# Kernel optimization log

Measured on AMD Instinct MI355X. Metric: run time of the kernel, lower is better.

## Reference

```python
import jax, jax.numpy as jnp
import numpy as np

N_QUBITS = 16
N_LAYERS = 4
DIM = 2 ** N_QUBITS  # 65536 == prod(input_size)


def rot_matrix(phi, theta, omega):
    # PennyLane Rot(phi, theta, omega) = RZ(omega) RY(theta) RZ(phi)
    c = jnp.cos(theta * 0.5).astype(jnp.complex64)
    s = jnp.sin(theta * 0.5).astype(jnp.complex64)
    ep = jnp.exp(-0.5j * (phi + omega).astype(jnp.complex64))  # e^{-i(phi+omega)/2}
    em = jnp.exp(0.5j * (phi - omega).astype(jnp.complex64))   # e^{ i(phi-omega)/2}
    return jnp.stack([
        jnp.stack([ep * c, -em * s]),
        jnp.stack([jnp.conj(em) * s, jnp.conj(ep) * c]),
    ])


def apply_1q(state, U, wire):
    # state: (batch, 2, 2, ..., 2); wire axis is 1 + wire (wire 0 = MSB, PennyLane convention)
    ax = 1 + wire
    s = jnp.moveaxis(state, ax, -1)
    s = jnp.einsum('...j,ij->...i', s, U)
    return jnp.moveaxis(s, -1, ax)


def apply_cnot(state, control, target):
    s = jnp.moveaxis(state, (1 + control, 1 + target), (-2, -1))
    # flip target amplitudes where control bit == 1
    s = jnp.concatenate([s[..., 0:1, :], s[..., 1:2, ::-1]], axis=-2)
    return jnp.moveaxis(s, (-2, -1), (1 + control, 1 + target))


def circuit_expvals(x, weights):
    batch = x.shape[0]
    x = x.reshape(batch, -1)  # (batch, 65536)
    # AmplitudeEmbedding with normalize=True (pad_with=0.0 is a no-op: exactly 2^16 features)
    norm = jnp.sqrt(jnp.sum(x * x, axis=1, keepdims=True))
    state = (x / norm).astype(jnp.complex64).reshape((batch,) + (2,) * N_QUBITS)
    # StronglyEntanglingLayers: per layer, Rot on every wire then a ring of CNOTs with range r
    for l in range(N_LAYERS):
        for w in range(N_QUBITS):
            U = rot_matrix(weights[l, w, 0], weights[l, w, 1], weights[l, w, 2])
            state = apply_1q(state, U, w)
        r = (l % (N_QUBITS - 1)) + 1  # PennyLane default ranges
        for w in range(N_QUBITS):
            state = apply_cnot(state, w, (w + r) % N_QUBITS)
    probs = (state.real ** 2 + state.imag ** 2)  # (batch, 2, ..., 2) float32
    z = []
    for w in range(N_QUBITS):
        p = jnp.moveaxis(probs, 1 + w, 1).reshape(batch, 2, -1).sum(-1)
        z.append(p[:, 0] - p[:, 1])  # <PauliZ(w)>
    return jnp.stack(z, axis=1)  # (batch, n_qubits)


def setup_inputs() -> dict:
    key = jax.random.key(0)
    k1, k2, k3, k4 = jax.random.split(key, 4)
    x = jax.random.normal(k1, (128, 256, 256), dtype=jnp.float32)
    # TorchLayer default init: uniform(0, 2*pi)
    weights = jax.random.uniform(k2, (N_LAYERS, N_QUBITS, 3), dtype=jnp.float32) * (2.0 * np.pi)
    # Linear(16, 2), xavier_uniform weight, default bias init (frozen but still used)
    bound = float(np.sqrt(6.0 / (N_QUBITS + 2)))
    c_weight = jax.random.uniform(k3, (2, N_QUBITS), dtype=jnp.float32, minval=-bound, maxval=bound)
    bb = float(1.0 / np.sqrt(N_QUBITS))
    c_bias = jax.random.uniform(k4, (2,), dtype=jnp.float32, minval=-bb, maxval=bb)
    return {"x": x, "weights": weights, "c_weight": c_weight, "c_bias": c_bias}


def reference(x, weights, c_weight, c_bias):
    expvals = circuit_expvals(x, weights)
    return expvals @ c_weight.T + c_bias  # (batch, 2)
```

## Files before the change

### kernel.cpp

```cpp
#include <hip/hip_runtime.h>
#include <cmath>
#include <utility>
#include <cstddef>


namespace qsim {

constexpr int NQ = 16;
constexpr int NL = 4;
constexpr int NGMAX = 12;
constexpr int GMAX  = 36;
constexpr int BDIM  = 13;
constexpr int CDIM  = 3;

constexpr int parity16(unsigned v) {
    int p = 0;
    for (int k = 0; k < 16; ++k) p ^= (int)((v >> k) & 1u);
    return p;
}
constexpr int topbit(unsigned v) {
    int b = -1;
    for (int k = 0; k < 16; ++k) if ((v >> k) & 1u) b = k;
    return b;
}

struct PlanT {
    int ngroups;
    int ng[NGMAX];
    unsigned char gl[NGMAX][GMAX];
    unsigned char gw[NGMAX][GMAX];
    unsigned short mloc[NGMAX][GMAX];
    unsigned short rloc[NGMAX][GMAX];
    unsigned short grow[NGMAX][GMAX];
    unsigned short V[NGMAX][BDIM];
    unsigned short U[NGMAX][CDIM];
    unsigned short frow[16];
    unsigned short floc[16];
    bool ok;
};

constexpr PlanT make_plan() {
    PlanT P{};
    P.ok = true;

    unsigned col[16] = {}, rowv[16] = {};
    for (int b = 0; b < 16; ++b) { col[b] = 1u << b; rowv[b] = 1u << b; }
    unsigned gmask[64] = {}, growg[64] = {};
    unsigned char glay[64] = {}, gwire[64] = {};
    int gi = 0;
    for (int l = 0; l < NL; ++l) {
        for (int w = 0; w < NQ; ++w) {
            const int b = 15 - w;
            gmask[gi] = col[b]; growg[gi] = rowv[b];
            glay[gi] = (unsigned char)l; gwire[gi] = (unsigned char)w; ++gi;
        }
        const int r = (l % (NQ - 1)) + 1;
        for (int w = 0; w < NQ; ++w) {
            const int cb = 15 - w;
            const int tb = 15 - ((w + r) % NQ);
            col[cb] ^= col[tb];
            rowv[tb] ^= rowv[cb];
        }
    }
    for (int b = 0; b < 16; ++b) P.frow[b] = (unsigned short)rowv[b];

    for (int a = 0; a < 16; ++a)
        for (int b2 = 0; b2 < 16; ++b2)
            if (parity16(rowv[a] & col[b2]) != (a == b2 ? 1 : 0)) P.ok = false;
    for (int i = 0; i < 64; ++i)
        if (parity16(gmask[i] & growg[i]) != 1) P.ok = false;

    bool applied[64] = {};
    int napplied = 0, grp = 0;
    while (napplied < 64) {
        if (grp >= NGMAX) { P.ok = false; break; }
        unsigned B[BDIM] = {}; int piv[BDIM] = {}; int nb = 0;
        for (int i = 0; i < 6; ++i) { B[i] = 1u << i; piv[i] = i; ++nb; }
        unsigned tmask[GMAX] = {}, trow[GMAX] = {};
        int cnt = 0;
        bool progress = true;
        while (progress) {
            progress = false;
            int lay = -1;
            for (int i = 0; i < 64; ++i)
                if (!applied[i]) { lay = glay[i]; break; }
            if (lay < 0) break;
            for (int w = 15; w >= 0; --w) {
                const int idx = lay * 16 + w;
                if (applied[idx]) continue;
                unsigned v = gmask[idx];
                for (int i = 0; i < nb; ++i) if ((v >> piv[i]) & 1u) v ^= B[i];
                if (v != 0u && nb == BDIM) continue;
                if (cnt >= GMAX) { P.ok = false; continue; }
                if (v != 0u) {
                    int pb = 0; while (((v >> pb) & 1u) == 0u) ++pb;
                    for (int i = 0; i < nb; ++i) if ((B[i] >> pb) & 1u) B[i] ^= v;
                    B[nb] = v; piv[nb] = pb; ++nb;
                }
                P.gl[grp][cnt] = glay[idx];
                P.gw[grp][cnt] = gwire[idx];
                tmask[cnt] = gmask[idx]; trow[cnt] = growg[idx];
                ++cnt;
                applied[idx] = true; ++napplied; progress = true;
            }
        }
        for (int bbit = 0; bbit < 16 && nb < BDIM; ++bbit) {
            unsigned v = 1u << bbit;
            for (int i = 0; i < nb; ++i) if ((v >> piv[i]) & 1u) v ^= B[i];
            if (v != 0u) {
                int pb = 0; while (((v >> pb) & 1u) == 0u) ++pb;
                for (int i = 0; i < nb; ++i) if ((B[i] >> pb) & 1u) B[i] ^= v;
                B[nb] = v; piv[nb] = pb; ++nb;
            }
        }
        if (nb != BDIM) P.ok = false;
        for (int i = 1; i < BDIM; ++i) {
            unsigned bv = B[i]; int pv = piv[i]; int j = i - 1;
            while (j >= 0 && B[j] > bv) { B[j+1] = B[j]; piv[j+1] = piv[j]; --j; }
            B[j+1] = bv; piv[j+1] = pv;
        }
        for (int i = 0; i < 6; ++i) if (B[i] != (1u << i)) P.ok = false;
        for (int i = 0; i < BDIM; ++i) P.V[grp][i] = (unsigned short)B[i];
        int cu = 0;
        for (int bbit = 0; bbit < 16; ++bbit) {
            bool isp = false;
            for (int i = 0; i < BDIM; ++i) if (piv[i] == bbit) isp = true;
            if (!isp) { if (cu < CDIM) P.U[grp][cu] = (unsigned short)(1u << bbit); ++cu; }
        }
        if (cu != CDIM) P.ok = false;
        for (int g = 0; g < cnt; ++g) {
            unsigned m = tmask[g], ml = 0;
            for (int i = 0; i < BDIM; ++i)
                if ((m >> piv[i]) & 1u) { ml |= 1u << i; m ^= B[i]; }
            if (m != 0u) P.ok = false;
            if (ml == 0u) P.ok = false;
            P.mloc[grp][g] = (unsigned short)ml;
            unsigned rl = 0;
            for (int i = 0; i < BDIM; ++i)
                rl |= (unsigned)parity16(trow[g] & B[i]) << i;
            P.rloc[grp][g] = (unsigned short)rl;
            P.grow[grp][g] = (unsigned short)trow[g];
        }
        P.ng[grp] = cnt;
        ++grp;
    }
    P.ngroups = grp;
    for (int q = 0; q < 16; ++q) {
        unsigned rl = 0;
        for (int s = 0; s < BDIM; ++s)
            rl |= (unsigned)parity16(P.frow[q] & P.V[P.ngroups - 1][s]) << s;
        P.floc[q] = (unsigned short)rl;
    }
    return P;
}

constexpr PlanT PLAN = make_plan();
static_assert(PLAN.ok, "constexpr plan construction failed");
static_assert(PLAN.ngroups >= 2 && PLAN.ngroups <= NGMAX, "unexpected group count");


__device__ __forceinline__ float xsgn(float v, unsigned sb) {
    return __uint_as_float(__float_as_uint(v) ^ sb);
}

template<int G>
__device__ __forceinline__ unsigned vmid(int tid) {
    unsigned rx = 0;
    if (tid & 64)  rx ^= PLAN.V[G][6];
    if (tid & 128) rx ^= PLAN.V[G][7];
    if (tid & 256) rx ^= PLAN.V[G][8];
    if (tid & 512) rx ^= PLAN.V[G][9];
    return rx;
}
template<int G>
__device__ __forceinline__ unsigned vhi(int j) {
    unsigned rx = 0;
    if (j & 1) rx ^= PLAN.V[G][10];
    if (j & 2) rx ^= PLAN.V[G][11];
    if (j & 4) rx ^= PLAN.V[G][12];
    return rx;
}

template<int G, int g>
__device__ __forceinline__ void apply_gates(float2* tile,
                                            const float* __restrict__ gu,
                                            unsigned base, int tid)
{
    if constexpr (g < PLAN.ng[G]) {
        constexpr unsigned ml  = PLAN.mloc[G][g];
        constexpr unsigned rl  = PLAN.rloc[G][g];
        constexpr unsigned grw = PLAN.grow[G][g];
        constexpr int gidx = PLAN.gl[G][g] * 16 + PLAN.gw[G][g];

        const float* up = gu + gidx * 8;
        const float u0r = up[0], u0i = up[1], u1r = up[2], u1i = up[3];
        const int pgb = __popc(grw & base) & 1;

        if constexpr (ml < 64u) {
            const int prt = (pgb ^ __popc(rl & (unsigned)tid)) & 1;
            #pragma unroll
            for (int j = 0; j < 8; ++j) {
                const int L = (j << 10) | tid;
                const float2 a = tile[L];
                const float bx = __shfl_xor(a.x, (int)ml, 64);
                const float by = __shfl_xor(a.y, (int)ml, 64);
                const int p = prt ^ (__popc(rl & ((unsigned)j << 10)) & 1);
                const unsigned sb = (unsigned)p << 31;
                const float say = xsgn(a.y, sb), sax = xsgn(a.x, sb);
                const float sbx = xsgn(bx, sb),  sby = xsgn(by, sb);
                float2 o;
                o.x = u0r*a.x - u0i*say + u1r*sbx - u1i*by;
                o.y = u0r*a.y + u0i*sax + u1r*sby + u1i*bx;
                tile[L] = o;
            }
        } else {
            constexpr int hb = topbit(ml);
            const unsigned etid = (((unsigned)tid >> hb) << (hb + 1)) |
                                  ((unsigned)tid & ((1u << hb) - 1u));
            const int ptid = (pgb ^ __popc(rl & etid)) & 1;
            #pragma unroll
            for (int j = 0; j < 4; ++j) {
                const unsigned cj = (unsigned)j << 10;
                const unsigned ej = ((cj >> hb) << (hb + 1)) |
                                    (cj & ((1u << hb) - 1u));
                const unsigned i = etid | ej;
                const unsigned k = i ^ ml;
                const float2 a = tile[i];
                const float2 b = tile[k];
                const int p = ptid ^ (__popc(rl & ej) & 1);
                const unsigned sb = (unsigned)p << 31;
                const float say = xsgn(a.y, sb), sax = xsgn(a.x, sb);
                const float sbx = xsgn(b.x, sb), sby = xsgn(b.y, sb);
                float2 oi, ok;
                oi.x = u0r*a.x - u0i*say + u1r*sbx - u1i*b.y;
                oi.y = u0r*a.y + u0i*sax + u1r*sby + u1i*b.x;
                ok.x = u0r*b.x + u0i*sby - u1r*sax - u1i*a.y;
                ok.y = u0r*b.y - u0i*sbx - u1r*say + u1i*a.x;
                tile[i] = oi; tile[k] = ok;
            }
        }
        constexpr bool cur_lane  = (ml < 64u);
        constexpr bool next_lane = (g + 1 < PLAN.ng[G]) &&
                                   (PLAN.mloc[G][g + 1] < 64u);
        constexpr bool last_gate = (g + 1 >= PLAN.ng[G]);
        if constexpr (!(cur_lane && (next_lane || last_gate))) __syncthreads();
        apply_gates<G, g + 1>(tile, gu, base, tid);
    }
}

template<int G, bool FIRST, bool LAST>
__global__ __launch_bounds__(1024, 8)
void pass_kernel(const float* __restrict__ x,
                 const float* __restrict__ gu,
                 float2* __restrict__ state,
                 const float* __restrict__ invn,
                 float* __restrict__ zpart)
{
    __shared__ float2 tile[1 << 13];
    const int tid = (int)threadIdx.x;
    const int batch = (int)blockIdx.x >> 3;
    const unsigned coset = (unsigned)blockIdx.x & 7u;

    unsigned base = 0;
    if (coset & 1u) base ^= PLAN.U[G][0];
    if (coset & 2u) base ^= PLAN.U[G][1];
    if (coset & 4u) base ^= PLAN.U[G][2];
    const unsigned gbt = base ^ (unsigned)(tid & 63) ^ vmid<G>(tid);
    const int boff = batch << 16;

    if constexpr (FIRST) {
        const float inv = invn[batch];
        #pragma unroll
        for (int j = 0; j < 8; ++j)
            tile[(j << 10) | tid] =
                make_float2(x[boff + (int)(gbt ^ vhi<G>(j))] * inv, 0.f);
    } else {
        #pragma unroll
        for (int j = 0; j < 8; ++j)
            tile[(j << 10) | tid] = state[boff + (int)(gbt ^ vhi<G>(j))];
    }
    if constexpr (!(PLAN.ng[G] > 0 && PLAN.mloc[G][0] < 64u)) __syncthreads();

    apply_gates<G, 0>(tile, gu, base, tid);

    if constexpr (LAST) {
        unsigned sbits = 0;
        #pragma unroll
        for (int q = 0; q < 16; ++q) {
            const int s0 = (__popc((unsigned)PLAN.frow[q] & base)
                          + __popc((unsigned)PLAN.floc[q] & (unsigned)tid)) & 1;
            sbits |= (unsigned)s0 << q;
        }
        const int wave = tid >> 6, lane = tid & 63;
        const int W = (int)blockIdx.x * 16 + wave;
        #pragma unroll
        for (int h = 0; h < 2; ++h) {
            float acc[8] = {0,0,0,0,0,0,0,0};
            #pragma unroll
            for (int j = 0; j < 8; ++j) {
                const float2 a = tile[(j << 10) | tid];
                const float pr = a.x*a.x + a.y*a.y;
                #pragma unroll
                for (int q8 = 0; q8 < 8; ++q8) {
                    const int q = h * 8 + q8;
                    const int s = (int)((sbits >> q) & 1u) ^
                        (__popc((unsigned)PLAN.floc[q] & ((unsigned)j << 10)) & 1);
                    acc[q8] += s ? -pr : pr;
                }
            }
            #pragma unroll
            for (int q8 = 0; q8 < 8; ++q8) {
                float v = acc[q8];
                #pragma unroll
                for (int o = 32; o; o >>= 1) v += __shfl_xor(v, o, 64);
                if (lane == 0) zpart[W * 16 + h * 8 + q8] = v;
            }
        }
    } else {
        #pragma unroll
        for (int j = 0; j < 8; ++j)
            state[boff + (int)(gbt ^ vhi<G>(j))] = tile[(j << 10) | tid];
    }
}

__global__ __launch_bounds__(256)
void norm_kernel(const float* __restrict__ x, float* __restrict__ invn)
{
    const int b = (int)blockIdx.x;
    const float4* xv = reinterpret_cast<const float4*>(x + ((size_t)b << 16));
    float s = 0.f;
    for (int i = (int)threadIdx.x; i < 16384; i += 256) {
        const float4 v = xv[i];
        s += v.x*v.x + v.y*v.y + v.z*v.z + v.w*v.w;
    }
    #pragma unroll
    for (int o = 32; o; o >>= 1) s += __shfl_xor(s, o, 64);
    __shared__ float partial[4];
    if ((threadIdx.x & 63u) == 0u) partial[threadIdx.x >> 6] = s;
    __syncthreads();
    if (threadIdx.x == 0) {
        const float t = partial[0] + partial[1] + partial[2] + partial[3];
        invn[b] = 1.0f / sqrtf(t);
    }
}

__global__ void gateu_kernel(const float* __restrict__ wts, float* __restrict__ gu)
{
    const int i = (int)threadIdx.x;
    if (i < 64) {
        const float phi = wts[i*3+0], th = wts[i*3+1], om = wts[i*3+2];
        float sh, ch; sincosf(0.5f * th, &sh, &ch);
        float sap, cap; sincosf(0.5f * (phi + om), &sap, &cap);
        float sam, cam; sincosf(0.5f * (phi - om), &sam, &cam);
        gu[i*8+0] =  cap*ch;  gu[i*8+1] = -sap*ch;
        gu[i*8+2] = -cam*sh;  gu[i*8+3] = -sam*sh;
        gu[i*8+4] =  cam*sh;  gu[i*8+5] = -sam*sh;
        gu[i*8+6] =  cap*ch;  gu[i*8+7] =  sap*ch;
    }
}

__global__ __launch_bounds__(1024)
void out_kernel(const float* __restrict__ zpart, const float* __restrict__ cw,
                const float* __restrict__ cb, float* __restrict__ out)
{
    const int b = (int)blockIdx.x;
    const int q = (int)(threadIdx.x >> 6);
    const int c = (int)(threadIdx.x & 63u);
    float v = zpart[(size_t)(((b << 7) | c) * 16 + q)]
            + zpart[(size_t)(((b << 7) | c | 64) * 16 + q)];
    #pragma unroll
    for (int o = 32; o; o >>= 1) v += __shfl_xor(v, o, 64);
    __shared__ float z[16];
    if (c == 0) z[q] = v;
    __syncthreads();
    if (threadIdx.x < 2) {
        const int o = (int)threadIdx.x;
        float acc = cb[o];
        #pragma unroll
        for (int w = 0; w < 16; ++w) acc += cw[o * 16 + w] * z[15 - w];
        out[b * 2 + o] = acc;
    }
}

__global__ void sentinel_kernel(float* out)
{
    if (threadIdx.x < 256) out[threadIdx.x] = -12345.0f;
}

template<int I>
static void launch_one(const float* x, const float* gu, float2* state,
                       const float* invn, float* zpart, hipStream_t s)
{
    pass_kernel<I, I == 0, I == PLAN.ngroups - 1>
        <<<1024, 1024, 0, s>>>(x, gu, state, invn, zpart);
}

template<std::size_t... I>
static void launch_all(std::index_sequence<I...>, const float* x, const float* gu,
                       float2* state, const float* invn, float* zpart, hipStream_t s)
{
    (launch_one<(int)I>(x, gu, state, invn, zpart, s), ...);
}

}

extern "C" void kernel_launch(void* const* d_in, const int* in_sizes, int n_in,
                              void* d_out, int out_size, void* d_ws, size_t ws_size,
                              hipStream_t stream)
{
    (void)in_sizes; (void)n_in; (void)out_size;
    const float* x   = (const float*)d_in[0];
    const float* wts = (const float*)d_in[1];
    const float* cw  = (const float*)d_in[2];
    const float* cb  = (const float*)d_in[3];
    float* out = (float*)d_out;

    constexpr size_t STATE_BYTES = (size_t)128 * 65536 * sizeof(float2);
    constexpr size_t INVN_OFF  = STATE_BYTES;
    constexpr size_t GATEU_OFF = STATE_BYTES + 1024;
    constexpr size_t ZPART_OFF = STATE_BYTES + 1024 + 4096;
    constexpr size_t ZPART_BYTES = (size_t)1024 * 16 * 16 * sizeof(float);
    constexpr size_t NEED = ZPART_OFF + ZPART_BYTES;

    if (ws_size < NEED) {
        qsim::sentinel_kernel<<<1, 256, 0, stream>>>(out);
        return;
    }

    float2* state = (float2*)d_ws;
    float* invn   = (float*)((char*)d_ws + INVN_OFF);
    float* gu     = (float*)((char*)d_ws + GATEU_OFF);
    float* zpart  = (float*)((char*)d_ws + ZPART_OFF);

    qsim::norm_kernel<<<128, 256, 0, stream>>>(x, invn);
    qsim::gateu_kernel<<<1, 64, 0, stream>>>(wts, gu);
    qsim::launch_all(std::make_index_sequence<(std::size_t)qsim::PLAN.ngroups>{},
                     x, gu, state, invn, zpart, stream);
    qsim::out_kernel<<<128, 1024, 0, stream>>>(zpart, cw, cb, out);
}
```

Before: 283.8 us.

## Keep amplitudes in registers and reorder basis slots to minimize LDS gates

```diff
diff --git a/kernel.cpp b/kernel.cpp
--- a/kernel.cpp
+++ b/kernel.cpp
@@ -17,11 +17,6 @@
     int p = 0;
     for (int k = 0; k < 16; ++k) p ^= (int)((v >> k) & 1u);
     return p;
-}
-constexpr int topbit(unsigned v) {
-    int b = -1;
-    for (int k = 0; k < 16; ++k) if ((v >> k) & 1u) b = k;
-    return b;
 }
 
 struct PlanT {
@@ -120,27 +115,49 @@
             B[j+1] = bv; piv[j+1] = pv;
         }
         for (int i = 0; i < 6; ++i) if (B[i] != (1u << i)) P.ok = false;
-        for (int i = 0; i < BDIM; ++i) P.V[grp][i] = (unsigned short)B[i];
-        int cu = 0;
-        for (int bbit = 0; bbit < 16; ++bbit) {
-            bool isp = false;
-            for (int i = 0; i < BDIM; ++i) if (piv[i] == bbit) isp = true;
-            if (!isp) { if (cu < CDIM) P.U[grp][cu] = (unsigned short)(1u << bbit); ++cu; }
-        }
-        if (cu != CDIM) P.ok = false;
+
+        unsigned provml[GMAX] = {};
         for (int g = 0; g < cnt; ++g) {
             unsigned m = tmask[g], ml = 0;
             for (int i = 0; i < BDIM; ++i)
                 if ((m >> piv[i]) & 1u) { ml |= 1u << i; m ^= B[i]; }
             if (m != 0u) P.ok = false;
             if (ml == 0u) P.ok = false;
-            P.mloc[grp][g] = (unsigned short)ml;
-            unsigned rl = 0;
+            provml[g] = ml;
+        }
+        int usage[BDIM] = {};
+        for (int g = 0; g < cnt; ++g)
+            for (int i = 6; i < BDIM; ++i)
+                if ((provml[g] >> i) & 1u) usage[i]++;
+        int ord[7] = {};
+        for (int k = 0; k < 7; ++k) ord[k] = 6 + k;
+        for (int i = 1; i < 7; ++i) {
+            int oi = ord[i]; int j = i - 1;
+            while (j >= 0 && usage[ord[j]] < usage[oi]) { ord[j+1] = ord[j]; --j; }
+            ord[j+1] = oi;
+        }
+        int slot[BDIM] = {};
+        for (int i = 0; i < 6; ++i) slot[i] = i;
+        for (int k = 0; k < 7; ++k) slot[ord[k]] = (k < 3) ? (10 + k) : (6 + (k - 3));
+        for (int i = 0; i < BDIM; ++i) P.V[grp][slot[i]] = (unsigned short)B[i];
+        for (int g = 0; g < cnt; ++g) {
+            unsigned ml2 = 0;
             for (int i = 0; i < BDIM; ++i)
-                rl |= (unsigned)parity16(trow[g] & B[i]) << i;
-            P.rloc[grp][g] = (unsigned short)rl;
+                if ((provml[g] >> i) & 1u) ml2 |= 1u << slot[i];
+            P.mloc[grp][g] = (unsigned short)ml2;
+            unsigned rlv = 0;
+            for (int s = 0; s < BDIM; ++s)
+                rlv |= (unsigned)parity16(trow[g] & P.V[grp][s]) << s;
+            P.rloc[grp][g] = (unsigned short)rlv;
             P.grow[grp][g] = (unsigned short)trow[g];
         }
+        int cu = 0;
+        for (int bbit = 0; bbit < 16; ++bbit) {
+            bool isp = false;
+            for (int i = 0; i < BDIM; ++i) if (piv[i] == bbit) isp = true;
+            if (!isp) { if (cu < CDIM) P.U[grp][cu] = (unsigned short)(1u << bbit); ++cu; }
+        }
+        if (cu != CDIM) P.ok = false;
         P.ng[grp] = cnt;
         ++grp;
     }
@@ -159,9 +176,7 @@
 static_assert(PLAN.ngroups >= 2 && PLAN.ngroups <= NGMAX, "unexpected group count");
 
 
-__device__ __forceinline__ float xsgn(float v, unsigned sb) {
-    return __uint_as_float(__float_as_uint(v) ^ sb);
-}
+constexpr unsigned WMASK = 0x3C0u;
 
 template<int G>
 __device__ __forceinline__ unsigned vmid(int tid) {
@@ -182,7 +197,8 @@
 }
 
 template<int G, int g>
-__device__ __forceinline__ void apply_gates(float2* tile,
+__device__ __forceinline__ void apply_gates(float2 (&a)[8],
+                                            float2* __restrict__ tile,
                                             const float* __restrict__ gu,
                                             unsigned base, int tid)
 {
@@ -191,60 +207,88 @@
         constexpr unsigned rl  = PLAN.rloc[G][g];
         constexpr unsigned grw = PLAN.grow[G][g];
         constexpr int gidx = PLAN.gl[G][g] * 16 + PLAN.gw[G][g];
+        constexpr unsigned lam = ml & 63u;
+        constexpr unsigned wm  = ml & WMASK;
+        constexpr unsigned jm  = (ml >> 10) & 7u;
 
         const float* up = gu + gidx * 8;
         const float u0r = up[0], u0i = up[1], u1r = up[2], u1i = up[3];
         const int pgb = __popc(grw & base) & 1;
-
-        if constexpr (ml < 64u) {
-            const int prt = (pgb ^ __popc(rl & (unsigned)tid)) & 1;
+        const int ptid = (pgb ^ __popc(rl & (unsigned)tid)) & 1;
+        const float a0i = ptid ? -u0i : u0i;
+        const float a1r = ptid ? -u1r : u1r;
+        const float b0i = -a0i, b1r = -a1r;
+
+        if constexpr (wm != 0u) {
+            #pragma unroll
+            for (int j = 0; j < 8; ++j) tile[(j << 10) | tid] = a[j];
+            __syncthreads();
             #pragma unroll
             for (int j = 0; j < 8; ++j) {
-                const int L = (j << 10) | tid;
-                const float2 a = tile[L];
-                const float bx = __shfl_xor(a.x, (int)ml, 64);
-                const float by = __shfl_xor(a.y, (int)ml, 64);
-                const int p = prt ^ (__popc(rl & ((unsigned)j << 10)) & 1);
-                const unsigned sb = (unsigned)p << 31;
-                const float say = xsgn(a.y, sb), sax = xsgn(a.x, sb);
-                const float sbx = xsgn(bx, sb),  sby = xsgn(by, sb);
+                const float2 p = tile[((j << 10) | tid) ^ (int)ml];
+                const int cj = __popc(rl & ((unsigned)j << 10)) & 1;
+                const float s0i = cj ? b0i : a0i, s1r = cj ? b1r : a1r;
                 float2 o;
-                o.x = u0r*a.x - u0i*say + u1r*sbx - u1i*by;
-                o.y = u0r*a.y + u0i*sax + u1r*sby + u1i*bx;
-                tile[L] = o;
+                o.x = u0r*a[j].x - s0i*a[j].y + s1r*p.x - u1i*p.y;
+                o.y = u0r*a[j].y + s0i*a[j].x + s1r*p.y + u1i*p.x;
+                a[j] = o;
+            }
+            __syncthreads();
+        } else if constexpr (jm == 0u) {
+            #pragma unroll
+            for (int j = 0; j < 8; ++j) {
+                const int cj = __popc(rl & ((unsigned)j << 10)) & 1;
+                const float s0i = cj ? b0i : a0i, s1r = cj ? b1r : a1r;
+                const float px = __shfl_xor(a[j].x, (int)lam, 64);
+                const float py = __shfl_xor(a[j].y, (int)lam, 64);
+                float2 o;
+                o.x = u0r*a[j].x - s0i*a[j].y + s1r*px - u1i*py;
+                o.y = u0r*a[j].y + s0i*a[j].x + s1r*py + u1i*px;
+                a[j] = o;
+            }
+        } else if constexpr (lam == 0u) {
+            constexpr unsigned lb = jm & (0u - jm);
+            #pragma unroll
+            for (int j = 0; j < 8; ++j) {
+                if ((j & (int)lb) == 0) {
+                    const int k = j ^ (int)jm;
+                    const int cj = __popc(rl & ((unsigned)j << 10)) & 1;
+                    const int ck = cj ^ 1;
+                    const float sj0 = cj ? b0i : a0i, sj1 = cj ? b1r : a1r;
+                    const float sk0 = ck ? b0i : a0i, sk1 = ck ? b1r : a1r;
+                    const float2 aj = a[j], ak = a[k];
+                    float2 oj, okv;
+                    oj.x = u0r*aj.x - sj0*aj.y + sj1*ak.x - u1i*ak.y;
+                    oj.y = u0r*aj.y + sj0*aj.x + sj1*ak.y + u1i*ak.x;
+                    okv.x = u0r*ak.x - sk0*ak.y + sk1*aj.x - u1i*aj.y;
+                    okv.y = u0r*ak.y + sk0*ak.x + sk1*aj.y + u1i*aj.x;
+                    a[j] = oj; a[k] = okv;
+                }
             }
         } else {
-            constexpr int hb = topbit(ml);
-            const unsigned etid = (((unsigned)tid >> hb) << (hb + 1)) |
-                                  ((unsigned)tid & ((1u << hb) - 1u));
-            const int ptid = (pgb ^ __popc(rl & etid)) & 1;
-            #pragma unroll
-            for (int j = 0; j < 4; ++j) {
-                const unsigned cj = (unsigned)j << 10;
-                const unsigned ej = ((cj >> hb) << (hb + 1)) |
-                                    (cj & ((1u << hb) - 1u));
-                const unsigned i = etid | ej;
-                const unsigned k = i ^ ml;
-                const float2 a = tile[i];
-                const float2 b = tile[k];
-                const int p = ptid ^ (__popc(rl & ej) & 1);
-                const unsigned sb = (unsigned)p << 31;
-                const float say = xsgn(a.y, sb), sax = xsgn(a.x, sb);
-                const float sbx = xsgn(b.x, sb), sby = xsgn(b.y, sb);
-                float2 oi, ok;
-                oi.x = u0r*a.x - u0i*say + u1r*sbx - u1i*b.y;
-                oi.y = u0r*a.y + u0i*sax + u1r*sby + u1i*b.x;
-                ok.x = u0r*b.x + u0i*sby - u1r*sax - u1i*a.y;
-                ok.y = u0r*b.y - u0i*sbx - u1r*say + u1i*a.x;
-                tile[i] = oi; tile[k] = ok;
-            }
-        }
-        constexpr bool cur_lane  = (ml < 64u);
-        constexpr bool next_lane = (g + 1 < PLAN.ng[G]) &&
-                                   (PLAN.mloc[G][g + 1] < 64u);
-        constexpr bool last_gate = (g + 1 >= PLAN.ng[G]);
-        if constexpr (!(cur_lane && (next_lane || last_gate))) __syncthreads();
-        apply_gates<G, g + 1>(tile, gu, base, tid);
+            constexpr unsigned lb = jm & (0u - jm);
+            #pragma unroll
+            for (int j = 0; j < 8; ++j) {
+                if ((j & (int)lb) == 0) {
+                    const int k = j ^ (int)jm;
+                    const float pjx = __shfl_xor(a[k].x, (int)lam, 64);
+                    const float pjy = __shfl_xor(a[k].y, (int)lam, 64);
+                    const float pkx = __shfl_xor(a[j].x, (int)lam, 64);
+                    const float pky = __shfl_xor(a[j].y, (int)lam, 64);
+                    const int cj = __popc(rl & ((unsigned)j << 10)) & 1;
+                    const int ck = __popc(rl & ((unsigned)k << 10)) & 1;
+                    const float sj0 = cj ? b0i : a0i, sj1 = cj ? b1r : a1r;
+                    const float sk0 = ck ? b0i : a0i, sk1 = ck ? b1r : a1r;
+                    float2 oj, okv;
+                    oj.x = u0r*a[j].x - sj0*a[j].y + sj1*pjx - u1i*pjy;
+                    oj.y = u0r*a[j].y + sj0*a[j].x + sj1*pjy + u1i*pjx;
+                    okv.x = u0r*a[k].x - sk0*a[k].y + sk1*pkx - u1i*pky;
+                    okv.y = u0r*a[k].y + sk0*a[k].x + sk1*pky + u1i*pkx;
+                    a[j] = oj; a[k] = okv;
+                }
+            }
+        }
+        apply_gates<G, g + 1>(a, tile, gu, base, tid);
     }
 }
 
@@ -268,20 +312,19 @@
     const unsigned gbt = base ^ (unsigned)(tid & 63) ^ vmid<G>(tid);
     const int boff = batch << 16;
 
+    float2 a[8];
     if constexpr (FIRST) {
         const float inv = invn[batch];
         #pragma unroll
         for (int j = 0; j < 8; ++j)
-            tile[(j << 10) | tid] =
-                make_float2(x[boff + (int)(gbt ^ vhi<G>(j))] * inv, 0.f);
+            a[j] = make_float2(x[boff + (int)(gbt ^ vhi<G>(j))] * inv, 0.f);
     } else {
         #pragma unroll
         for (int j = 0; j < 8; ++j)
-            tile[(j << 10) | tid] = state[boff + (int)(gbt ^ vhi<G>(j))];
-    }
-    if constexpr (!(PLAN.ng[G] > 0 && PLAN.mloc[G][0] < 64u)) __syncthreads();
-
-    apply_gates<G, 0>(tile, gu, base, tid);
+            a[j] = state[boff + (int)(gbt ^ vhi<G>(j))];
+    }
+
+    apply_gates<G, 0>(a, tile, gu, base, tid);
 
     if constexpr (LAST) {
         unsigned sbits = 0;
@@ -298,8 +341,7 @@
             float acc[8] = {0,0,0,0,0,0,0,0};
             #pragma unroll
             for (int j = 0; j < 8; ++j) {
-                const float2 a = tile[(j << 10) | tid];
-                const float pr = a.x*a.x + a.y*a.y;
+                const float pr = a[j].x*a[j].x + a[j].y*a[j].y;
                 #pragma unroll
                 for (int q8 = 0; q8 < 8; ++q8) {
                     const int q = h * 8 + q8;
@@ -319,7 +361,7 @@
     } else {
         #pragma unroll
         for (int j = 0; j < 8; ++j)
-            state[boff + (int)(gbt ^ vhi<G>(j))] = tile[(j << 10) | tid];
+            state[boff + (int)(gbt ^ vhi<G>(j))] = a[j];
     }
 }
 
```

Result: slower. 384.7 us (+35.6%).
